# Kernel optimization log

Hardware: AMD Instinct MI355X
Metric: run time of the kernel (lower is better)

Reference implementation:

```python
import jax, jax.numpy as jnp
import numpy as np

S, E, H, D, F = 2048, 1280, 16, 80, 5120
EPS = 1e-6


def _ln(x, g, b):
    m = x.mean(-1, keepdims=True)
    v = x.var(-1, keepdims=True)
    return (x - m) * jax.lax.rsqrt(v + EPS) * g + b


def _rotate_half(x):
    x1, x2 = jnp.split(x, 2, axis=-1)
    return jnp.concatenate([-x2, x1], axis=-1)


def _quick_gelu(x):
    return x * jax.nn.sigmoid(1.702 * x)


def setup_inputs() -> dict:
    key = jax.random.key(0)
    ks = jax.random.split(key, 12)
    inp = {
        "hidden_states": jax.random.normal(ks[0], (S, E), jnp.float32),
        "attention_mask": jnp.ones((1, 1, S, S), jnp.bool_),
        "cos": jax.random.uniform(ks[1], (S, D), jnp.float32),
        "sin": jax.random.uniform(ks[2], (S, D), jnp.float32),
        "ln1_g": jnp.ones((E,), jnp.float32),
        "ln1_b": jnp.zeros((E,), jnp.float32),
        "ln2_g": jnp.ones((E,), jnp.float32),
        "ln2_b": jnp.zeros((E,), jnp.float32),
        "w_qkv": jax.random.normal(ks[3], (E, 3 * E), jnp.float32) * (E ** -0.5),
        "b_qkv": jax.random.normal(ks[4], (3 * E,), jnp.float32) * 0.02,
        "w_o": jax.random.normal(ks[5], (E, E), jnp.float32) * (E ** -0.5),
        "b_o": jax.random.normal(ks[6], (E,), jnp.float32) * 0.02,
        "w_fc1": jax.random.normal(ks[7], (E, F), jnp.float32) * (E ** -0.5),
        "b_fc1": jax.random.normal(ks[8], (F,), jnp.float32) * 0.02,
        "w_fc2": jax.random.normal(ks[9], (F, E), jnp.float32) * (F ** -0.5),
        "b_fc2": jax.random.normal(ks[10], (E,), jnp.float32) * 0.02,
    }
    return inp


def reference(hidden_states, attention_mask, cos, sin, ln1_g, ln1_b, ln2_g, ln2_b,
              w_qkv, b_qkv, w_o, b_o, w_fc1, b_fc1, w_fc2, b_fc2):
    x = hidden_states  # [S, E]
    h = _ln(x, ln1_g, ln1_b)
    qkv = h @ w_qkv + b_qkv  # [S, 3E]
    q, k, v = jnp.split(qkv, 3, axis=-1)
    q = q.reshape(S, H, D)
    k = k.reshape(S, H, D)
    v = v.reshape(S, H, D)
    # rotary in fp32, cos/sin broadcast over head axis: [S, 1, D]
    c = cos[:, None, :].astype(jnp.float32)
    s = sin[:, None, :].astype(jnp.float32)
    qf, kf = q.astype(jnp.float32), k.astype(jnp.float32)
    q = (qf * c + _rotate_half(qf) * s).astype(q.dtype)
    k = (kf * c + _rotate_half(kf) * s).astype(k.dtype)
    # attention scores [H, S, S]
    scores = jnp.einsum('shd,thd->hst', q, k) / np.float32(np.sqrt(D))
    scores = jnp.where(attention_mask[0], scores, jnp.finfo(scores.dtype).min)
    probs = jax.nn.softmax(scores.astype(jnp.float32), axis=-1).astype(q.dtype)
    attn = jnp.einsum('hst,thd->shd', probs, v).reshape(S, E)
    attn = attn @ w_o + b_o
    x = x + attn
    h2 = _ln(x, ln2_g, ln2_b)
    mlp = _quick_gelu(h2 @ w_fc1 + b_fc1) @ w_fc2 + b_fc2
    return x + mlp
```

## Files before the change

### kernel.cpp

```cpp
#include <hip/hip_runtime.h>
#include <stdint.h>
#include <math.h>

#define S_LEN 2048
#define EMB   1280
#define NHEAD 16
#define HDIM  80
#define FDIM  5120

typedef __bf16 bf16x8 __attribute__((ext_vector_type(8)));
typedef float  f32x4  __attribute__((ext_vector_type(4)));
typedef int    i32x4  __attribute__((ext_vector_type(4)));
typedef unsigned short u16x8 __attribute__((ext_vector_type(8)));
typedef unsigned short u16x4 __attribute__((ext_vector_type(4)));

__device__ __forceinline__ float b2f(unsigned short u) {
    union { float f; unsigned int i; } x; x.i = ((unsigned int)u) << 16; return x.f;
}
__device__ __forceinline__ unsigned short f2b(float f) {
    union { float f; unsigned int i; } x; x.f = f;
    unsigned int r = x.i + 0x7FFFu + ((x.i >> 16) & 1u);
    return (unsigned short)(r >> 16);
}

__device__ __forceinline__ float wave_rsum(float v) {
    #pragma unroll
    for (int o = 32; o; o >>= 1) v += __shfl_down(v, o);
    return v;
}

__device__ __forceinline__ void gload16(const unsigned short* g, unsigned short* l) {
    __builtin_amdgcn_global_load_lds(
        (const __attribute__((address_space(1))) void*)g,
        (__attribute__((address_space(3))) void*)l, 16, 0, 0);
}

__device__ __forceinline__ void trans64(
    const float* __restrict__ in, unsigned short* __restrict__ out,
    int R, int C, int bx, int by, int tid)
{
    __shared__ unsigned short tile[64][65];
    int c0 = bx * 64, r0 = by * 64;
    int tx = tid & 63, ty = tid >> 6;
    #pragma unroll
    for (int j = 0; j < 16; ++j) {
        int row = ty + j * 4;
        tile[row][tx] = f2b(in[(size_t)(r0 + row) * C + c0 + tx]);
    }
    __syncthreads();
    #pragma unroll
    for (int j = 0; j < 16; ++j) {
        int row = ty + j * 4;
        out[(size_t)(c0 + row) * R + r0 + tx] = tile[tx][row];
    }
}

__global__ __launch_bounds__(256) void transpose4_kernel(
    const float* __restrict__ w_qkv, unsigned short* __restrict__ wT_qkv,
    const float* __restrict__ w_o,   unsigned short* __restrict__ wT_o,
    const float* __restrict__ w_fc1, unsigned short* __restrict__ wT_fc1,
    const float* __restrict__ w_fc2, unsigned short* __restrict__ wT_fc2)
{
    int id = blockIdx.x, tid = threadIdx.x;
    if (id < 1200) {
        trans64(w_qkv, wT_qkv, 1280, 3840, id % 60, id / 60, tid);
    } else if (id < 1600) {
        int t = id - 1200;
        trans64(w_o, wT_o, 1280, 1280, t % 20, t / 20, tid);
    } else if (id < 3200) {
        int t = id - 1600;
        trans64(w_fc1, wT_fc1, 1280, 5120, t % 80, t / 80, tid);
    } else {
        int t = id - 3200;
        trans64(w_fc2, wT_fc2, 5120, 1280, t % 20, t / 20, tid);
    }
}

__global__ __launch_bounds__(256) void ln_kernel(
    const float* __restrict__ x,
    const float* __restrict__ g,
    const float* __restrict__ b,
    unsigned short* __restrict__ out)
{
    int row = blockIdx.x, tid = threadIdx.x;
    int lane = tid & 63, wave = tid >> 6;
    const float* xr = x + (size_t)row * EMB;
    float v[5], s = 0.f, ss = 0.f;
    #pragma unroll
    for (int i = 0; i < 5; ++i) {
        float f = xr[tid + i * 256];
        v[i] = f; s += f; ss += f * f;
    }
    s = wave_rsum(s); ss = wave_rsum(ss);
    __shared__ float rs[4], rss[4];
    if (lane == 0) { rs[wave] = s; rss[wave] = ss; }
    __syncthreads();
    float st  = rs[0] + rs[1] + rs[2] + rs[3];
    float sst = rss[0] + rss[1] + rss[2] + rss[3];
    float mean = st * (1.0f / EMB);
    float var  = sst * (1.0f / EMB) - mean * mean;
    float inv  = rsqrtf(var + 1e-6f);
    unsigned short* orow = out + (size_t)row * EMB;
    #pragma unroll
    for (int i = 0; i < 5; ++i) {
        int c = tid + i * 256;
        orow[c] = f2b((v[i] - mean) * inv * g[c] + b[c]);
    }
}

template<int EPI, int OM, int SPLIT>
__global__ __launch_bounds__(256) void gemm_kernel(
    const unsigned short* __restrict__ A,
    const unsigned short* __restrict__ Bt,
    const float* __restrict__ bias,
    const float* __restrict__ res,
    void* __restrict__ Cv,
    int M, int N, int K)
{
    __shared__ __align__(16) unsigned short As[2][128 * 32];
    __shared__ __align__(16) unsigned short Bs[2][128 * 32];

    int tid = threadIdx.x;
    int lane = tid & 63, wave = tid >> 6;
    int m0 = blockIdx.x * 128, n0 = blockIdx.y * 128;
    int wm = (wave >> 1) * 64, wn = (wave & 1) * 64;
    int kc = K / SPLIT;
    int kbeg = blockIdx.z * kc;
    const int NITER = kc / 32;

    f32x4 acc[4][4];
    #pragma unroll
    for (int i = 0; i < 4; ++i)
        #pragma unroll
        for (int j = 0; j < 4; ++j)
            acc[i][j] = (f32x4){0.f, 0.f, 0.f, 0.f};

    int u = tid ^ ((tid >> 3) & 7);
    const unsigned short* Ap0 = A  + (size_t)(m0 + (u >> 2)) * K + (u & 3) * 8 + kbeg;
    const unsigned short* Ap1 = Ap0 + (size_t)64 * K;
    const unsigned short* Bp0 = Bt + (size_t)(n0 + (u >> 2)) * K + (u & 3) * 8 + kbeg;
    const unsigned short* Bp1 = Bp0 + (size_t)64 * K;

    int arow = lane & 15, aq = (lane >> 4) * 8;
    int aswz = ((arow >> 1) & 7) << 3;
    int aoff[4], boff[4];
    #pragma unroll
    for (int i = 0; i < 4; ++i) {
        aoff[i] = ((wm + i * 16 + arow) * 32 + aq) ^ aswz;
        boff[i] = ((wn + i * 16 + arow) * 32 + aq) ^ aswz;
    }

    int wbase = wave * 512;

#define STAGE(B, KO)                                                          \
    {                                                                         \
        gload16(Ap0 + (KO), &As[B][wbase]);                                   \
        gload16(Ap1 + (KO), &As[B][2048 + wbase]);                            \
        gload16(Bp0 + (KO), &Bs[B][wbase]);                                   \
        gload16(Bp1 + (KO), &Bs[B][2048 + wbase]);                            \
    }

    STAGE(0, 0)
    __syncthreads();

    for (int it = 0; it < NITER; ++it) {
        int cur = it & 1;
        if (it + 1 < NITER) STAGE(cur ^ 1, (it + 1) * 32)
        bf16x8 af[4], bfm[4];
        #pragma unroll
        for (int i = 0; i < 4; ++i) {
            af[i]  = *(const bf16x8*)&As[cur][aoff[i]];
            bfm[i] = *(const bf16x8*)&Bs[cur][boff[i]];
        }
        #pragma unroll
        for (int mi = 0; mi < 4; ++mi)
            #pragma unroll
            for (int ni = 0; ni < 4; ++ni)
                acc[mi][ni] = __builtin_amdgcn_mfma_f32_16x16x32_bf16(
                    af[mi], bfm[ni], acc[mi][ni], 0, 0, 0);
        __syncthreads();
    }
#undef STAGE

    int col = lane & 15;
    int rbase = (lane >> 4) * 4;
    #pragma unroll
    for (int ni = 0; ni < 4; ++ni) {
        int gn = n0 + wn + ni * 16 + col;
        float bv = (OM == 2) ? 0.f : bias[gn];
        #pragma unroll
        for (int mi = 0; mi < 4; ++mi) {
            int gm = m0 + wm + mi * 16 + rbase;
            #pragma unroll
            for (int r = 0; r < 4; ++r) {
                float v = acc[mi][ni][r] + bv;
                if (OM != 2) {
                    if (EPI == 1) v = v / (1.0f + expf(-1.702f * v));
                }
                if (OM == 2)
                    ((float*)Cv)[((size_t)blockIdx.z * M + gm + r) * N + gn] = v;
                else if (OM == 1)
                    ((float*)Cv)[(size_t)(gm + r) * N + gn] = v;
                else
                    ((unsigned short*)Cv)[(size_t)(gm + r) * N + gn] = f2b(v);
            }
        }
    }
}

template<int Z>
__global__ __launch_bounds__(256) void reduceZ_kernel(
    const float* __restrict__ part,
    const float* __restrict__ res,
    const float* __restrict__ bias,
    float* __restrict__ out)
{
    size_t i4 = ((size_t)blockIdx.x * 256 + threadIdx.x) * 4;
    int colb = (int)(i4 % EMB);
    f32x4 a = *(const f32x4*)&res[i4];
    f32x4 bv = *(const f32x4*)&bias[colb];
    a += bv;
    const size_t slice = (size_t)S_LEN * EMB;
    #pragma unroll
    for (int z = 0; z < Z; ++z)
        a += *(const f32x4*)&part[z * slice + i4];
    *(f32x4*)&out[i4] = a;
}

__global__ __launch_bounds__(256) void ropev_kernel(
    const unsigned short* __restrict__ qkv,
    const float* __restrict__ cosb,
    const float* __restrict__ sinb,
    unsigned short* __restrict__ q_out,
    unsigned short* __restrict__ k_out,
    unsigned short* __restrict__ vt)
{
    __shared__ unsigned short qT[64 * 84];
    __shared__ unsigned short kT[64 * 84];
    __shared__ unsigned short vT[64 * 84];

    int h = blockIdx.x >> 5, stile = blockIdx.x & 31;
    int s0 = stile * 64;
    int tid = threadIdx.x;

    u16x4 qr[5], kr[5];
    #pragma unroll
    for (int i = 0; i < 5; ++i) {
        int u = tid + i * 256;
        int row = u / 20, col = (u % 20) * 4;
        const unsigned short* base = qkv + (size_t)(s0 + row) * (3 * EMB) + h * HDIM + col;
        qr[i] = *(const u16x4*)base;
        kr[i] = *(const u16x4*)(base + EMB);
        u16x4 v4 = *(const u16x4*)(base + 2 * EMB);
        *(u16x4*)&qT[row * 84 + col] = qr[i];
        *(u16x4*)&kT[row * 84 + col] = kr[i];
        *(u16x4*)&vT[row * 84 + col] = v4;
    }
    __syncthreads();

    #pragma unroll
    for (int i = 0; i < 5; ++i) {
        int u = tid + i * 256;
        int row = u / 20, col = (u % 20) * 4;
        int pcol = (col < 40) ? col + 40 : col - 40;
        float sgn = (col < 40) ? -1.f : 1.f;
        u16x4 qp = *(const u16x4*)&qT[row * 84 + pcol];
        u16x4 kp = *(const u16x4*)&kT[row * 84 + pcol];
        f32x4 c4 = *(const f32x4*)&cosb[(size_t)(s0 + row) * HDIM + col];
        f32x4 s4 = *(const f32x4*)&sinb[(size_t)(s0 + row) * HDIM + col];
        u16x4 qo, ko;
        #pragma unroll
        for (int j = 0; j < 4; ++j) {
            qo[j] = f2b(b2f(qr[i][j]) * c4[j] + sgn * b2f(qp[j]) * s4[j]);
            ko[j] = f2b(b2f(kr[i][j]) * c4[j] + sgn * b2f(kp[j]) * s4[j]);
        }
        size_t o = ((size_t)h * S_LEN + s0 + row) * HDIM + col;
        *(u16x4*)&q_out[o] = qo;
        *(u16x4*)&k_out[o] = ko;
    }
    #pragma unroll
    for (int i = 0; i < 5; ++i) {
        int w = tid + i * 256;
        int d = w >> 4, c4i = (w & 15) * 4;
        u16x4 pk;
        #pragma unroll
        for (int j = 0; j < 4; ++j) pk[j] = vT[(c4i + j) * 84 + d];
        *(u16x4*)(vt + ((size_t)h * HDIM + d) * S_LEN + s0 + c4i) = pk;
    }
}

__global__ __launch_bounds__(256) void fattn_kernel(
    const unsigned short* __restrict__ q,
    const unsigned short* __restrict__ k,
    const unsigned short* __restrict__ vt,
    unsigned short* __restrict__ out)
{
    __shared__ __align__(16) unsigned short Ks[2][64 * 96];
    __shared__ __align__(16) unsigned short Vs[2][80 * 72];
    __shared__ __align__(16) unsigned short Pt[4 * 16 * 72];

    int tid = threadIdx.x;
    int lane = tid & 63, wave = tid >> 6;
    int arow = lane & 15, quad = lane >> 4;
    int h = blockIdx.x >> 5, qb = blockIdx.x & 31;
    int s0 = qb * 64;
    const float c = 0.16129856f;

    const unsigned short* kbase = k + (size_t)h * S_LEN * HDIM;
    const unsigned short* vbase = vt + (size_t)h * HDIM * S_LEN;

    bf16x8 qf[3];
    {
        const unsigned short* qrp =
            q + ((size_t)h * S_LEN + s0 + wave * 16 + arow) * HDIM;
        #pragma unroll
        for (int kk = 0; kk < 3; ++kk) {
            int col = kk * 32 + quad * 8;
            u16x8 qv = (u16x8){0, 0, 0, 0, 0, 0, 0, 0};
            if (col < HDIM) qv = *(const u16x8*)(qrp + col);
            u16x8 qs8;
            #pragma unroll
            for (int j = 0; j < 8; ++j) qs8[j] = f2b(b2f(qv[j]) * c);
            qf[kk] = *(bf16x8*)&qs8;
        }
    }

    {
        int zr = tid >> 2, zc = 80 + (tid & 3) * 4;
        int zidx = (zr * 96 + zc) ^ ((zr & 7) << 3);
        *(u16x4*)&Ks[0][zidx] = (u16x4){0, 0, 0, 0};
        *(u16x4*)&Ks[1][zidx] = (u16x4){0, 0, 0, 0};
    }

    u16x4 kreg[5], vreg[5];
    #pragma unroll
    for (int i = 0; i < 5; ++i) {
        int u = tid + i * 256;
        kreg[i] = *(const u16x4*)(kbase + u * 4);
        vreg[i] = *(const u16x4*)(vbase + (size_t)(u >> 4) * S_LEN + (u & 15) * 4);
    }
    #pragma unroll
    for (int i = 0; i < 5; ++i) {
        int u = tid + i * 256;
        int row = u / 20, c4 = (u % 20) * 4;
        *(u16x4*)&Ks[0][(row * 96 + c4) ^ ((row & 7) << 3)] = kreg[i];
        *(u16x4*)&Vs[0][(u >> 4) * 72 + (u & 15) * 4] = vreg[i];
    }
    #pragma unroll
    for (int i = 0; i < 5; ++i) {
        int u = tid + i * 256;
        kreg[i] = *(const u16x4*)(kbase + (size_t)64 * HDIM + u * 4);
        vreg[i] = *(const u16x4*)(vbase + (size_t)(u >> 4) * S_LEN + 64 + (u & 15) * 4);
    }
    __syncthreads();

    int ksw[3];
    #pragma unroll
    for (int kk = 0; kk < 3; ++kk)
        ksw[kk] = (arow * 96 + kk * 32 + quad * 8) ^ ((arow & 7) << 3);

    int pw = wave * 16 * 72;
    int poff = pw + arow * 72 + ((arow >> 3) << 2);

    float l_part = 0.f;
    f32x4 o[5];
    #pragma unroll
    for (int di = 0; di < 5; ++di) o[di] = (f32x4){0.f, 0.f, 0.f, 0.f};

    const int NIT = S_LEN / 64;
    for (int it = 0; it < NIT; ++it) {
        int cur = it & 1;
        if (it + 1 < NIT) {
            int nb = (it + 1) & 1;
            #pragma unroll
            for (int i = 0; i < 5; ++i) {
                int u = tid + i * 256;
                int row = u / 20, c4 = (u % 20) * 4;
                *(u16x4*)&Ks[nb][(row * 96 + c4) ^ ((row & 7) << 3)] = kreg[i];
                *(u16x4*)&Vs[nb][(u >> 4) * 72 + (u & 15) * 4] = vreg[i];
            }
        }
        if (it + 2 < NIT) {
            int t0 = (it + 2) * 64;
            #pragma unroll
            for (int i = 0; i < 5; ++i) {
                int u = tid + i * 256;
                kreg[i] = *(const u16x4*)(kbase + (size_t)t0 * HDIM + u * 4);
                vreg[i] = *(const u16x4*)(vbase + (size_t)(u >> 4) * S_LEN + t0 + (u & 15) * 4);
            }
        }

        f32x4 sc[4];
        #pragma unroll
        for (int ni = 0; ni < 4; ++ni) sc[ni] = (f32x4){0.f, 0.f, 0.f, 0.f};
        __builtin_amdgcn_s_setprio(1);
        #pragma unroll
        for (int kk = 0; kk < 3; ++kk) {
            bf16x8 bq = qf[kk];
            #pragma unroll
            for (int ni = 0; ni < 4; ++ni) {
                bf16x8 ak = *(const bf16x8*)&Ks[cur][ksw[kk] + ni * 1536];
                sc[ni] = __builtin_amdgcn_mfma_f32_16x16x32_bf16(ak, bq, sc[ni], 0, 0, 0);
            }
        }
        __builtin_amdgcn_s_setprio(0);

        #pragma unroll
        for (int ni = 0; ni < 4; ++ni) {
            u16x4 pk;
            #pragma unroll
            for (int r = 0; r < 4; ++r) {
                float p = __builtin_amdgcn_exp2f(sc[ni][r]);
                l_part += p;
                __bf16 pb = (__bf16)p;
                pk[r] = *(unsigned short*)&pb;
            }
            *(u16x4*)&Pt[poff + ni * 16 + quad * 4] = pk;
        }

        __builtin_amdgcn_s_setprio(1);
        #pragma unroll
        for (int kk = 0; kk < 2; ++kk) {
            u16x4 plo = *(const u16x4*)&Pt[poff + kk * 32 + quad * 8];
            u16x4 phi = *(const u16x4*)&Pt[poff + kk * 32 + quad * 8 + 4];
            u16x8 apu = (u16x8){plo[0], plo[1], plo[2], plo[3],
                                phi[0], phi[1], phi[2], phi[3]};
            bf16x8 ap = *(bf16x8*)&apu;
            #pragma unroll
            for (int di = 0; di < 5; ++di) {
                bf16x8 bv = *(const bf16x8*)&Vs[cur][(di * 16 + arow) * 72 + kk * 32 + quad * 8];
                o[di] = __builtin_amdgcn_mfma_f32_16x16x32_bf16(ap, bv, o[di], 0, 0, 0);
            }
        }
        __builtin_amdgcn_s_setprio(0);

        __syncthreads();
    }

    float l_run = l_part;
    l_run += __shfl_xor(l_run, 16);
    l_run += __shfl_xor(l_run, 32);

    float inv[4];
    #pragma unroll
    for (int r = 0; r < 4; ++r)
        inv[r] = 1.f / __shfl(l_run, (lane & 48) | (quad * 4 + r));
    #pragma unroll
    for (int r = 0; r < 4; ++r) {
        int gq = s0 + wave * 16 + quad * 4 + r;
        unsigned short* op = out + (size_t)gq * EMB + h * HDIM;
        #pragma unroll
        for (int di = 0; di < 5; ++di)
            op[di * 16 + arow] = f2b(o[di][r] * inv[r]);
    }
}

extern "C" void kernel_launch(void* const* d_in, const int* in_sizes, int n_in,
                              void* d_out, int out_size, void* d_ws, size_t ws_size,
                              hipStream_t stream)
{
    const float* hidden = (const float*)d_in[0];
    const float* cosb  = (const float*)d_in[2];
    const float* sinb  = (const float*)d_in[3];
    const float* ln1g  = (const float*)d_in[4];
    const float* ln1b  = (const float*)d_in[5];
    const float* ln2g  = (const float*)d_in[6];
    const float* ln2b  = (const float*)d_in[7];
    const float* w_qkv = (const float*)d_in[8];
    const float* b_qkv = (const float*)d_in[9];
    const float* w_o   = (const float*)d_in[10];
    const float* b_o   = (const float*)d_in[11];
    const float* w_fc1 = (const float*)d_in[12];
    const float* b_fc1 = (const float*)d_in[13];
    const float* w_fc2 = (const float*)d_in[14];
    const float* b_fc2 = (const float*)d_in[15];

    char* ws = (char*)d_ws;
    size_t off = 0;
    auto alloc = [&](size_t bytes) -> void* {
        void* p = (void*)(ws + off);
        off += (bytes + 255) & ~(size_t)255;
        return p;
    };
    unsigned short* wT_qkv = (unsigned short*)alloc((size_t)3840 * 1280 * 2);
    unsigned short* wT_o   = (unsigned short*)alloc((size_t)1280 * 1280 * 2);
    unsigned short* wT_fc1 = (unsigned short*)alloc((size_t)5120 * 1280 * 2);
    unsigned short* wT_fc2 = (unsigned short*)alloc((size_t)1280 * 5120 * 2);
    unsigned short* h1     = (unsigned short*)alloc((size_t)S_LEN * EMB * 2);
    unsigned short* qkv    = (unsigned short*)alloc((size_t)S_LEN * 3 * EMB * 2);
    unsigned short* q_r    = (unsigned short*)alloc((size_t)S_LEN * EMB * 2);
    unsigned short* k_r    = (unsigned short*)alloc((size_t)S_LEN * EMB * 2);
    unsigned short* vt_g   = (unsigned short*)alloc((size_t)S_LEN * EMB * 2);
    unsigned short* attn_o = (unsigned short*)alloc((size_t)S_LEN * EMB * 2);
    float*          x1     = (float*)alloc((size_t)S_LEN * EMB * 4);
    unsigned short* h2     = (unsigned short*)alloc((size_t)S_LEN * EMB * 2);
    unsigned short* mlp1   = (unsigned short*)alloc((size_t)S_LEN * FDIM * 2);
    float* partials = (float*)h1;

    transpose4_kernel<<<4800, 256, 0, stream>>>(
        w_qkv, wT_qkv, w_o, wT_o, w_fc1, wT_fc1, w_fc2, wT_fc2);

    ln_kernel<<<S_LEN, 256, 0, stream>>>(hidden, ln1g, ln1b, h1);

    gemm_kernel<0, 0, 1><<<dim3(S_LEN / 128, 3840 / 128, 1), 256, 0, stream>>>(
        h1, wT_qkv, b_qkv, nullptr, qkv, S_LEN, 3 * EMB, EMB);

    ropev_kernel<<<NHEAD * (S_LEN / 64), 256, 0, stream>>>(qkv, cosb, sinb, q_r, k_r, vt_g);

    fattn_kernel<<<NHEAD * (S_LEN / 64), 256, 0, stream>>>(q_r, k_r, vt_g, attn_o);

    gemm_kernel<0, 2, 2><<<dim3(S_LEN / 128, 1280 / 128, 2), 256, 0, stream>>>(
        attn_o, wT_o, b_o, nullptr, partials, S_LEN, EMB, EMB);
    reduceZ_kernel<2><<<(S_LEN * EMB / 4) / 256, 256, 0, stream>>>(
        partials, hidden, b_o, x1);

    ln_kernel<<<S_LEN, 256, 0, stream>>>(x1, ln2g, ln2b, h2);

    gemm_kernel<1, 0, 1><<<dim3(S_LEN / 128, FDIM / 128, 1), 256, 0, stream>>>(
        h2, wT_fc1, b_fc1, nullptr, mlp1, S_LEN, FDIM, EMB);

    gemm_kernel<0, 2, 4><<<dim3(S_LEN / 128, 1280 / 128, 4), 256, 0, stream>>>(
        mlp1, wT_fc2, b_fc2, nullptr, partials, S_LEN, EMB, FDIM);
    reduceZ_kernel<4><<<(S_LEN * EMB / 4) / 256, 256, 0, stream>>>(
        partials, x1, b_fc2, (float*)d_out);
}
```

Before: 369.8 us.

## Deepen GEMM LDS pipeline to four stages and remap blocks across XCDs

The GEMM mainloop moves from a double-buffered LDS scheme with a full __syncthreads per iteration to a 4-slot ring. Loads are issued three tiles ahead, and each iteration waits with explicit partial s_waitcnt vmcnt plus s_barrier, so global loads stay in flight behind the MFMAs. It also remaps the flat workgroup id so that consecutive logical tiles land on the same XCD (grouping by id mod 8), which should improve L2 reuse. The cost is twice the LDS (64KB per block), which may lower occupancy. The remap assumes the block count is divisible by 8.

Measured after the change: 376.6 us. Within noise of the previous version (+1.8%).

```diff
diff --git a/kernel.cpp b/kernel.cpp
--- a/kernel.cpp
+++ b/kernel.cpp
@@ -117,15 +117,26 @@
     void* __restrict__ Cv,
     int M, int N, int K)
 {
-    __shared__ __align__(16) unsigned short As[2][128 * 32];
-    __shared__ __align__(16) unsigned short Bs[2][128 * 32];
+    __shared__ __align__(16) unsigned short As[4][128 * 32];
+    __shared__ __align__(16) unsigned short Bs[4][128 * 32];
 
     int tid = threadIdx.x;
     int lane = tid & 63, wave = tid >> 6;
-    int m0 = blockIdx.x * 128, n0 = blockIdx.y * 128;
+
+    int gx = gridDim.x, gy = gridDim.y;
+    int nwg = gx * gy * gridDim.z;
+    int flat = blockIdx.x + gx * (blockIdx.y + gy * blockIdx.z);
+    int cpx = nwg >> 3;
+    int logical = (flat & 7) * cpx + (flat >> 3);
+    int bx = logical % gx;
+    int rem = logical / gx;
+    int by = rem % gy;
+    int bz = rem / gy;
+
+    int m0 = bx * 128, n0 = by * 128;
     int wm = (wave >> 1) * 64, wn = (wave & 1) * 64;
     int kc = K / SPLIT;
-    int kbeg = blockIdx.z * kc;
+    int kbeg = bz * kc;
     const int NITER = kc / 32;
 
     f32x4 acc[4][4];
@@ -159,28 +170,39 @@
         gload16(Bp0 + (KO), &Bs[B][wbase]);                                   \
         gload16(Bp1 + (KO), &Bs[B][2048 + wbase]);                            \
     }
+#define WAITB(N)                                                              \
+    asm volatile("s_waitcnt vmcnt(" #N ")\n\ts_barrier" ::: "memory");
 
     STAGE(0, 0)
-    __syncthreads();
+    if (NITER > 1) STAGE(1, 32)
+    if (NITER > 2) STAGE(2, 64)
+    if (NITER > 2)      { WAITB(8) }
+    else if (NITER > 1) { WAITB(4) }
+    else                { WAITB(0) }
 
     for (int it = 0; it < NITER; ++it) {
-        int cur = it & 1;
-        if (it + 1 < NITER) STAGE(cur ^ 1, (it + 1) * 32)
+        int cur = it & 3;
         bf16x8 af[4], bfm[4];
         #pragma unroll
         for (int i = 0; i < 4; ++i) {
             af[i]  = *(const bf16x8*)&As[cur][aoff[i]];
             bfm[i] = *(const bf16x8*)&Bs[cur][boff[i]];
         }
+        if (it + 3 < NITER) STAGE((it + 3) & 3, (it + 3) * 32)
         #pragma unroll
         for (int mi = 0; mi < 4; ++mi)
             #pragma unroll
             for (int ni = 0; ni < 4; ++ni)
                 acc[mi][ni] = __builtin_amdgcn_mfma_f32_16x16x32_bf16(
                     af[mi], bfm[ni], acc[mi][ni], 0, 0, 0);
-        __syncthreads();
+        if (it + 1 < NITER) {
+            if (it + 3 < NITER)      { WAITB(8) }
+            else if (it + 2 < NITER) { WAITB(4) }
+            else                     { WAITB(0) }
+        }
     }
 #undef STAGE
+#undef WAITB
 
     int col = lane & 15;
     int rbase = (lane >> 4) * 4;
@@ -198,7 +220,7 @@
                     if (EPI == 1) v = v / (1.0f + expf(-1.702f * v));
                 }
                 if (OM == 2)
-                    ((float*)Cv)[((size_t)blockIdx.z * M + gm + r) * N + gn] = v;
+                    ((float*)Cv)[((size_t)bz * M + gm + r) * N + gn] = v;
                 else if (OM == 1)
                     ((float*)Cv)[(size_t)(gm + r) * N + gn] = v;
                 else
```
